# Kernel tuning notes

Measured on AMD Instinct MI355X. Metric: run time of the kernel, lower is better.

## Reference

```python
import jax, jax.numpy as jnp
import numpy as np

RANK, A1, A2, B1, B2, BATCH = 16, 64, 8, 64, 8, 32768

def setup_inputs() -> dict:
    key = jax.random.key(0)
    kx, ks, ka, kb, kbias = jax.random.split(key, 5)
    # Params drawn as small gaussians (stand-in for xavier init; exact init
    x = jax.random.normal(kx, (BATCH, A1 * B1), dtype=jnp.float32)
    s = jax.random.normal(ks, (A1, A2), dtype=jnp.float32)
    a = jax.random.normal(ka, (RANK, A1, A2), dtype=jnp.float32) * 0.05
    b = jax.random.normal(kb, (RANK, B1, B2), dtype=jnp.float32) * 0.05
    bias = jax.random.normal(kbias, (A2 * B2,), dtype=jnp.float32)
    return {"x": x, "s": s, "a": a, "b": b, "bias": bias}

def reference(x, s, a, b, bias):
    # sa[r] = s * a[r]   (elementwise scale shared across ranks)
    sa = s[None, :, :] * a                                    # (r, a1, a2)
    # w = sum_r kron(sa[r], b[r]): w[i*b1+k, j*b2+l] = sum_r sa[r,i,j] b[r,k,l]
    # w is only (a1*b1, a2*b2) = (4096, 64), cheap to materialize here.
    w = jnp.einsum('rij,rkl->ikjl', sa, b).reshape(A1 * B1, A2 * B2)
    return x @ w + bias[None, :]                              # (batch, a2*b2)
```

## Files before the change

### kernel.cpp

```cpp
#include <hip/hip_runtime.h>
#include <hip/hip_bf16.h>

#define RANK 16
#define BATCH 32768
#define K_DIM 4096
#define N_DIM 64
#define CHUNK 256
#define NCHUNK 16
#define ROWB 32

typedef __bf16 bf16x8 __attribute__((ext_vector_type(8)));
typedef float floatx4 __attribute__((ext_vector_type(4)));
typedef unsigned short ushort8 __attribute__((ext_vector_type(8)));

#define WAITVM(n) asm volatile("s_waitcnt vmcnt(" #n ")" ::: "memory")
#define BARRIER() asm volatile("s_barrier" ::: "memory")

__device__ inline unsigned short f2bf(float f) {
  unsigned u = __builtin_bit_cast(unsigned, f);
  u += 0x7fffu + ((u >> 16) & 1u);
  return (unsigned short)(u >> 16);
}

__device__ inline bf16x8 cvt8(float4 a0, float4 a1) {
  ushort8 au;
  au[0] = f2bf(a0.x); au[1] = f2bf(a0.y); au[2] = f2bf(a0.z); au[3] = f2bf(a0.w);
  au[4] = f2bf(a1.x); au[5] = f2bf(a1.y); au[6] = f2bf(a1.z); au[7] = f2bf(a1.w);
  return __builtin_bit_cast(bf16x8, au);
}

__global__ __launch_bounds__(256) void build_wF(
    const float* __restrict__ s, const float* __restrict__ a,
    const float* __restrict__ b, unsigned short* __restrict__ wF) {
  int e = blockIdx.x * 256 + threadIdx.x;
  int j    = e & 7;
  int lane = (e >> 3) & 63;
  int ks   = (e >> 9) & 127;
  int cg   = e >> 16;
  int n = cg * 16 + (lane & 15);
  int k = ks * 32 + ((lane >> 4) << 3) + j;
  int i = k >> 6, kk = k & 63, jj = n >> 3, ll = n & 7;
  float acc = 0.f;
  #pragma unroll
  for (int r = 0; r < RANK; ++r) {
    acc += a[r * 512 + i * 8 + jj] * b[r * 512 + kk * 8 + ll];
  }
  acc *= s[i * 8 + jj];
  wF[e] = f2bf(acc);
}

__global__ __launch_bounds__(256, 2) void kron_gemm(
    const float* __restrict__ x, const unsigned short* __restrict__ wF,
    const float* __restrict__ bias, float* __restrict__ out) {
  __shared__ __align__(16) float As[2][ROWB * CHUNK];

  const int tid  = threadIdx.x;
  const int lane = tid & 63;
  const int wave = tid >> 6;
  const int ln15 = lane & 15;
  const int kseg = lane >> 4;
  const int m0   = blockIdx.x * ROWB;
  const int swl  = lane << 4;

  floatx4 acc[2] = {};

  struct W8 { bf16x8 t[8]; };

  auto loadw = [&](int c) {
    W8 w;
    #pragma unroll
    for (int t = 0; t < 8; ++t)
      w.t[t] = *(const bf16x8*)(wF + (((size_t)(wave * 128 + c * 8 + t)) << 9)
                                + (lane << 3));
    return w;
  };

  auto stage = [&](float* buf, int c) {
    #pragma unroll
    for (int p = 0; p < 8; ++p) {
      const int row = wave * 8 + p;
      const int sb  = swl ^ ((row & 7) << 4);
      const float* src = x + (size_t)(m0 + row) * K_DIM + c * CHUNK + (sb >> 2);
      float* dst = buf + row * CHUNK;
      __builtin_amdgcn_global_load_lds(
          (const __attribute__((address_space(1))) void*)(const void*)src,
          (__attribute__((address_space(3))) void*)(void*)dst, 16, 0, 0);
    }
  };

  auto compute = [&](const float* buf, const W8& w) {
    const char* Ab = (const char*)buf;
    #pragma unroll
    for (int t = 0; t < 8; ++t) {
      #pragma unroll
      for (int f = 0; f < 2; ++f) {
        const int row = f * 16 + ln15;
        const int swz = (row & 7) << 4;
        const int b0  = t * 128 + kseg * 32;
        float4 lo = *(const float4*)(Ab + row * 1024 + ((b0)      ^ swz));
        float4 hi = *(const float4*)(Ab + row * 1024 + ((b0 + 16) ^ swz));
        acc[f] = __builtin_amdgcn_mfma_f32_16x16x32_bf16(cvt8(lo, hi), w.t[t],
                                                         acc[f], 0, 0, 0);
      }
    }
  };

  float* A0 = &As[0][0];
  float* A1 = &As[1][0];

  W8 wA = loadw(0);
  stage(A0, 0);

  #pragma unroll 1
  for (int i = 0; i < 7; ++i) {
    const int c = 2 * i;
    W8 wB = loadw(c + 1);
    stage(A1, c + 1);
    WAITVM(16);
    BARRIER();
    compute(A0, wA);
    BARRIER();

    wA = loadw(c + 2);
    stage(A0, c + 2);
    WAITVM(16);
    BARRIER();
    compute(A1, wB);
    BARRIER();
  }
  {
    W8 wB = loadw(15);
    stage(A1, 15);
    WAITVM(16);
    BARRIER();
    compute(A0, wA);
    BARRIER();
    WAITVM(0);
    BARRIER();
    compute(A1, wB);
  }

  const int col = wave * 16 + ln15;
  const float bv = bias[col];
  #pragma unroll
  for (int f = 0; f < 2; ++f) {
    float* op = out + (size_t)(m0 + f * 16 + kseg * 4) * N_DIM + col;
    #pragma unroll
    for (int r = 0; r < 4; ++r)
      op[(size_t)r * N_DIM] = acc[f][r] + bv;
  }
}

extern "C" void kernel_launch(void* const* d_in, const int* in_sizes, int n_in,
                              void* d_out, int out_size, void* d_ws, size_t ws_size,
                              hipStream_t stream) {
  const float* x    = (const float*)d_in[0];
  const float* s    = (const float*)d_in[1];
  const float* a    = (const float*)d_in[2];
  const float* b    = (const float*)d_in[3];
  const float* bias = (const float*)d_in[4];
  float* out = (float*)d_out;
  unsigned short* wF = (unsigned short*)d_ws;

  build_wF<<<1024, 256, 0, stream>>>(s, a, b, wF);
  kron_gemm<<<BATCH / ROWB, 256, 0, stream>>>(x, wF, bias, out);
}
```

Baseline: 140.2 us.

## Convert x to bf16 before LDS, double block rows, stage output through LDS

Replaces direct global-to-LDS fp32 staging with register loads of x that are converted to bf16 once and written to a rotated LDS layout. MFMA operands then come straight from LDS without per-compute conversion. The row block doubles to 64 rows with four accumulators, which halves the number of redundant W loads per row. Output is staged through LDS for coalesced float4 stores. This costs more registers (16 float4 prefetch per thread), which risks lower occupancy, and the pipeline now waits on all outstanding loads (vmcnt 0) before each LDS write.

```diff
diff --git a/kernel.cpp b/kernel.cpp
--- a/kernel.cpp
+++ b/kernel.cpp
@@ -7,26 +7,20 @@
 #define N_DIM 64
 #define CHUNK 256
 #define NCHUNK 16
-#define ROWB 32
+#define ROWB 64
 
 typedef __bf16 bf16x8 __attribute__((ext_vector_type(8)));
 typedef float floatx4 __attribute__((ext_vector_type(4)));
-typedef unsigned short ushort8 __attribute__((ext_vector_type(8)));
+typedef unsigned short bfu4 __attribute__((ext_vector_type(4)));
 
-#define WAITVM(n) asm volatile("s_waitcnt vmcnt(" #n ")" ::: "memory")
-#define BARRIER() asm volatile("s_barrier" ::: "memory")
+#define WAITVM(n)  asm volatile("s_waitcnt vmcnt(" #n ")" ::: "memory")
+#define WAITLGKM() asm volatile("s_waitcnt lgkmcnt(0)" ::: "memory")
+#define BARRIER()  asm volatile("s_barrier" ::: "memory")
 
 __device__ inline unsigned short f2bf(float f) {
   unsigned u = __builtin_bit_cast(unsigned, f);
   u += 0x7fffu + ((u >> 16) & 1u);
   return (unsigned short)(u >> 16);
-}
-
-__device__ inline bf16x8 cvt8(float4 a0, float4 a1) {
-  ushort8 au;
-  au[0] = f2bf(a0.x); au[1] = f2bf(a0.y); au[2] = f2bf(a0.z); au[3] = f2bf(a0.w);
-  au[4] = f2bf(a1.x); au[5] = f2bf(a1.y); au[6] = f2bf(a1.z); au[7] = f2bf(a1.w);
-  return __builtin_bit_cast(bf16x8, au);
 }
 
 __global__ __launch_bounds__(256) void build_wF(
@@ -52,7 +46,7 @@
 __global__ __launch_bounds__(256, 2) void kron_gemm(
     const float* __restrict__ x, const unsigned short* __restrict__ wF,
     const float* __restrict__ bias, float* __restrict__ out) {
-  __shared__ __align__(16) float As[2][ROWB * CHUNK];
+  __shared__ __align__(16) __bf16 As[2][ROWB * CHUNK];
 
   const int tid  = threadIdx.x;
   const int lane = tid & 63;
@@ -60,11 +54,11 @@
   const int ln15 = lane & 15;
   const int kseg = lane >> 4;
   const int m0   = blockIdx.x * ROWB;
-  const int swl  = lane << 4;
 
-  floatx4 acc[2] = {};
+  floatx4 acc[4] = {};
 
-  struct W8 { bf16x8 t[8]; };
+  struct W8  { bf16x8 t[8]; };
+  struct X16 { float4 v[16]; };
 
   auto loadw = [&](int c) {
     W8 w;
@@ -75,79 +69,96 @@
     return w;
   };
 
-  auto stage = [&](float* buf, int c) {
+  auto loadx = [&](int c) {
+    X16 xv;
     #pragma unroll
-    for (int p = 0; p < 8; ++p) {
-      const int row = wave * 8 + p;
-      const int sb  = swl ^ ((row & 7) << 4);
-      const float* src = x + (size_t)(m0 + row) * K_DIM + c * CHUNK + (sb >> 2);
-      float* dst = buf + row * CHUNK;
-      __builtin_amdgcn_global_load_lds(
-          (const __attribute__((address_space(1))) void*)(const void*)src,
-          (__attribute__((address_space(3))) void*)(void*)dst, 16, 0, 0);
+    for (int j = 0; j < 16; ++j)
+      xv.v[j] = *(const float4*)(x + (size_t)(m0 + wave * 16 + j) * K_DIM
+                                 + c * CHUNK + 4 * lane);
+    return xv;
+  };
+
+  auto writeAs = [&](int buf, const X16& xv) {
+    char* Ab = (char*)&As[buf][0];
+    const int u    = lane >> 1;
+    const int half = lane & 1;
+    #pragma unroll
+    for (int j = 0; j < 16; ++j) {
+      bfu4 o;
+      o[0] = f2bf(xv.v[j].x); o[1] = f2bf(xv.v[j].y);
+      o[2] = f2bf(xv.v[j].z); o[3] = f2bf(xv.v[j].w);
+      const int phys = (u + 2 * j) & 31;
+      *(bfu4*)(Ab + (wave * 16 + j) * 512 + phys * 16 + half * 8) = o;
     }
   };
 
-  auto compute = [&](const float* buf, const W8& w) {
-    const char* Ab = (const char*)buf;
+  auto compute = [&](int buf, const W8& w) {
+    const char* Ab = (const char*)&As[buf][0];
     #pragma unroll
     for (int t = 0; t < 8; ++t) {
       #pragma unroll
-      for (int f = 0; f < 2; ++f) {
-        const int row = f * 16 + ln15;
-        const int swz = (row & 7) << 4;
-        const int b0  = t * 128 + kseg * 32;
-        float4 lo = *(const float4*)(Ab + row * 1024 + ((b0)      ^ swz));
-        float4 hi = *(const float4*)(Ab + row * 1024 + ((b0 + 16) ^ swz));
-        acc[f] = __builtin_amdgcn_mfma_f32_16x16x32_bf16(cvt8(lo, hi), w.t[t],
+      for (int f = 0; f < 4; ++f) {
+        const int row  = f * 16 + ln15;
+        const int phys = (4 * t + kseg + 2 * ln15) & 31;
+        bf16x8 af = *(const bf16x8*)(Ab + row * 512 + phys * 16);
+        acc[f] = __builtin_amdgcn_mfma_f32_16x16x32_bf16(af, w.t[t],
                                                          acc[f], 0, 0, 0);
       }
     }
   };
 
-  float* A0 = &As[0][0];
-  float* A1 = &As[1][0];
-
   W8 wA = loadw(0);
-  stage(A0, 0);
+  X16 xA = loadx(0);
+  WAITVM(0);
+  writeAs(0, xA);
+  W8 wB = loadw(1);
+  xA = loadx(1);
+  WAITLGKM();
+  BARRIER();
 
   #pragma unroll 1
   for (int i = 0; i < 7; ++i) {
     const int c = 2 * i;
-    W8 wB = loadw(c + 1);
-    stage(A1, c + 1);
-    WAITVM(16);
-    BARRIER();
-    compute(A0, wA);
+    compute(0, wA);
+    WAITVM(0);
+    writeAs(1, xA);
+    wA = loadw(c + 2);
+    xA = loadx(c + 2);
+    WAITLGKM();
     BARRIER();
 
-    wA = loadw(c + 2);
-    stage(A0, c + 2);
-    WAITVM(16);
-    BARRIER();
-    compute(A1, wB);
+    compute(1, wB);
+    WAITVM(0);
+    writeAs(0, xA);
+    wB = loadw(c + 3);
+    xA = loadx(c + 3);
+    WAITLGKM();
     BARRIER();
   }
-  {
-    W8 wB = loadw(15);
-    stage(A1, 15);
-    WAITVM(16);
-    BARRIER();
-    compute(A0, wA);
-    BARRIER();
-    WAITVM(0);
-    BARRIER();
-    compute(A1, wB);
-  }
+  compute(0, wA);
+  WAITVM(0);
+  writeAs(1, xA);
+  WAITLGKM();
+  BARRIER();
+  compute(1, wB);
 
+  BARRIER();
+  float* A0 = (float*)&As[0][0];
   const int col = wave * 16 + ln15;
   const float bv = bias[col];
   #pragma unroll
-  for (int f = 0; f < 2; ++f) {
-    float* op = out + (size_t)(m0 + f * 16 + kseg * 4) * N_DIM + col;
+  for (int f = 0; f < 4; ++f) {
     #pragma unroll
     for (int r = 0; r < 4; ++r)
-      op[(size_t)r * N_DIM] = acc[f][r] + bv;
+      A0[(f * 16 + kseg * 4 + r) * N_DIM + col] = acc[f][r] + bv;
+  }
+  __syncthreads();
+  float4* og = (float4*)(out + (size_t)m0 * N_DIM);
+  const float4* ol = (const float4*)A0;
+  #pragma unroll
+  for (int p = 0; p < 4; ++p) {
+    const int fi = p * 256 + tid;
+    og[fi] = ol[fi];
   }
 }
 
```

Measured after the change: 138.7 us. No clear change (-1.1%).
